# Optimization experiments

Hardware: AMD Instinct MI355X
Metric: run time of the kernel (lower is better)

Reference implementation:

```python
import jax, jax.numpy as jnp
import numpy as np
import math


def _sinusoidal_pe(seq_len, hidden_dim, dtype):
    pos = jnp.arange(seq_len, dtype=jnp.float32)[:, None]              # [S,1]
    div = jnp.exp(jnp.arange(0, hidden_dim, 2, dtype=jnp.float32) * (-math.log(10000.0) / hidden_dim))  # [H/2]
    ang = pos * div                                                    # [S,H/2]
    pe = jnp.stack([jnp.sin(ang), jnp.cos(ang)], axis=-1).reshape(seq_len, hidden_dim)  # interleave sin/cos
    return pe.astype(dtype)


def setup_inputs() -> dict:
    key = jax.random.key(0)
    ks = jax.random.split(key, 12)
    B, S, H = 4, 2048, 1024
    scale = 1.0 / math.sqrt(H)
    inp = {
        "x": jax.random.normal(ks[0], (B, S, H), dtype=jnp.float32),
        "mask": jax.random.randint(ks[1], (B, S, S), 0, 2, dtype=jnp.int32),
        "Wq": jax.random.normal(ks[2], (H, H), dtype=jnp.float32) * scale,
        "bq": jax.random.normal(ks[3], (H,), dtype=jnp.float32) * 0.02,
        "Wk": jax.random.normal(ks[4], (H, H), dtype=jnp.float32) * scale,
        "bk": jax.random.normal(ks[5], (H,), dtype=jnp.float32) * 0.02,
        "Wv": jax.random.normal(ks[6], (H, H), dtype=jnp.float32) * scale,
        "bv": jax.random.normal(ks[7], (H,), dtype=jnp.float32) * 0.02,
        "pos_bias": jax.random.normal(ks[8], (S, S), dtype=jnp.float32),
        "Wo": jax.random.normal(ks[9], (H, H), dtype=jnp.float32) * scale,
        "bo": jax.random.normal(ks[10], (H,), dtype=jnp.float32) * 0.02,
        "gamma": jnp.ones((H,), dtype=jnp.float32),
        "beta": jnp.zeros((H,), dtype=jnp.float32),
    }
    return inp


def reference(x, mask, Wq, bq, Wk, bk, Wv, bv, pos_bias, Wo, bo, gamma, beta):
    B, S, H = x.shape
    scale = math.sqrt(H)
    pe = _sinusoidal_pe(S, H, x.dtype)                  # [S,H]
    xp = x + pe[None, :, :]                             # [B,S,H]
    # torch Linear: y = x @ W.T + b
    q = jnp.einsum('bsh,oh->bso', xp, Wq) + bq
    k = jnp.einsum('bsh,oh->bso', xp, Wk) + bk
    v = jnp.einsum('bsh,oh->bso', xp, Wv) + bv
    scores = jnp.einsum('bqh,bkh->bqk', q, k) / scale   # [B,S,S]
    scores = scores + pos_bias[None, :S, :S]
    scores = jnp.where(mask == 0, jnp.asarray(-1e9, scores.dtype), scores)
    attn = jax.nn.softmax(scores, axis=-1)              # dropout = identity (eval mode)
    context = jnp.einsum('bqk,bkh->bqh', attn, v)
    out = jnp.einsum('bsh,oh->bso', context, Wo) + bo
    # LayerNorm(out + x)
    h = out + x
    mu = jnp.mean(h, axis=-1, keepdims=True)
    var = jnp.var(h, axis=-1, keepdims=True)
    normed = (h - mu) * jax.lax.rsqrt(var + 1e-5) * gamma + beta
    return normed, attn
```

## Files before the change

### kernel.cpp

```cpp
#include <hip/hip_runtime.h>
#include <hip/hip_bf16.h>
#include <math.h>

typedef __hip_bfloat16 bf16;
typedef __bf16 bf16x8 __attribute__((ext_vector_type(8)));
typedef float f32x4 __attribute__((ext_vector_type(4)));

static constexpr int  B_  = 4, S_ = 2048, H_ = 1024;
static constexpr long BSH = (long)B_ * S_ * H_;
static constexpr long SH  = (long)S_ * H_;
static constexpr long SS  = (long)S_ * S_;
static constexpr long HH  = (long)H_ * H_;

#define GLOAD_LDS16(gp, lp)                                                          \
  __builtin_amdgcn_global_load_lds((__attribute__((address_space(1))) void*)(gp),    \
                                   (__attribute__((address_space(3))) void*)(lp),    \
                                   16, 0, 0)

#define BARRIER() do { __builtin_amdgcn_s_barrier(); asm volatile("" ::: "memory"); } while (0)

template <int N> __device__ __forceinline__ void waitcnt_vm() {
  if constexpr (N == 0)      asm volatile("s_waitcnt vmcnt(0)" ::: "memory");
  else if constexpr (N == 8) asm volatile("s_waitcnt vmcnt(8)" ::: "memory");
}

__device__ __forceinline__ float wave_reduce_sum(float v) {
#pragma unroll
  for (int o = 32; o; o >>= 1) v += __shfl_xor(v, o, 64);
  return v;
}
__device__ __forceinline__ float bf16r(float v) {
  return __bfloat162float(__float2bfloat16(v));
}


__device__ __forceinline__ void prep_core(
    int bx, const float* Wq, const float* Wk, const float* Wv, const float* Wo,
    bf16* wdst, const float* x, bf16* xpb,
    const int* mask, unsigned* mask_bits, const float* pos_bias, bf16* pbb) {
  const int tid = threadIdx.x;
  if (bx < 4096) {
    const int w = bx >> 10;
    const float* src = (w == 0) ? Wq : (w == 1) ? Wk : (w == 2) ? Wv : Wo;
    bf16* d = wdst + (long)w * HH;
    const int idx = ((bx & 1023) << 8) + tid;
    const float4 f = ((const float4*)src)[idx];
    d[idx * 4 + 0] = __float2bfloat16(f.x);
    d[idx * 4 + 1] = __float2bfloat16(f.y);
    d[idx * 4 + 2] = __float2bfloat16(f.z);
    d[idx * 4 + 3] = __float2bfloat16(f.w);
  } else if (bx < 20480) {
    const long idx = (((long)(bx - 4096)) << 8) + tid;
    const int  i   = (int)(idx & (H_ / 2 - 1));
    const long bs  = idx >> 9;
    const int  s   = (int)(bs & (S_ - 1));
    const float div = __expf((float)(2 * i) * (-9.210340371976184f / (float)H_));
    const float ang = (float)s * div;
    const float2 xv = ((const float2*)x)[idx];
    xpb[idx * 2 + 0] = __float2bfloat16(xv.x + __sinf(ang));
    xpb[idx * 2 + 1] = __float2bfloat16(xv.y + __cosf(ang));
  } else if (bx < 22528) {
    const long uidx = (((long)(bx - 20480)) << 8) + tid;
    const int4* mp  = (const int4*)mask + uidx * 8;
    unsigned bits = 0;
#pragma unroll
    for (int q = 0; q < 8; ++q) {
      const int4 v = mp[q];
      bits |= (v.x ? 1u : 0u) << (q * 4 + 0);
      bits |= (v.y ? 1u : 0u) << (q * 4 + 1);
      bits |= (v.z ? 1u : 0u) << (q * 4 + 2);
      bits |= (v.w ? 1u : 0u) << (q * 4 + 3);
    }
    mask_bits[uidx] = bits;
  } else {
    const long idx = (((long)(bx - 22528)) << 8) + tid;
    const float4 f = ((const float4*)pos_bias)[idx];
    bf16* d = pbb + idx * 4;
    d[0] = __float2bfloat16(f.x);
    d[1] = __float2bfloat16(f.y);
    d[2] = __float2bfloat16(f.z);
    d[3] = __float2bfloat16(f.w);
  }
}

template <int MODE, bool DBUF>
__device__ __forceinline__ void gemm_core(
    bf16* As, bf16* Bs, int bxx, int byy, int z,
    const bf16* A, long sA, const bf16* Bm, long sB,
    bf16* Cb, float* Cf, long sC, int M, int N, int K,
    const float* bias0, const float* bias1,
    const bf16* pbb, const unsigned* mask_bits,
    const float* xres, const float* inv_sum) {
  constexpr int BM = 128, BN = 128, BK = 64;
  constexpr int TILE = BM * BK;

  const int tid  = threadIdx.x;
  const int lane = tid & 63;
  const int wave = tid >> 6;
  const int wm   = wave & 1;
  const int wn   = wave >> 1;
  const int m0   = bxx * BM;
  const int n0   = byy * BN;

  const bf16* Ab = A  + (long)z * sA;
  const bf16* Bb = Bm + (long)z * sB;

  const int rw = tid >> 3;
  const int cp = (tid & 7) ^ (rw & 7);
  const bf16* ga = Ab + (long)(m0 + rw) * K + cp * 8;
  const bf16* gb = Bb + (long)(n0 + rw) * K + cp * 8;

  auto stage = [&](int tile, int buf) {
    const long k0 = (long)tile * BK;
#pragma unroll
    for (int q = 0; q < 4; ++q) {
      GLOAD_LDS16(ga + (long)(32 * q) * K + k0, As + buf * TILE + tid * 8 + q * 2048);
      GLOAD_LDS16(gb + (long)(32 * q) * K + k0, Bs + buf * TILE + tid * 8 + q * 2048);
    }
  };

  f32x4 acc[4][4] = {};

  const int fr     = lane & 15;
  const int k0slot = lane >> 4;
  const int sw     = fr & 7;

  auto tile_compute = [&](const char* bAc, const char* bBc) {
#pragma unroll
    for (int ks = 0; ks < 2; ++ks) {
      const int co = ((k0slot + 4 * ks) ^ sw) << 4;
      bf16x8 af[4], bfv[4];
#pragma unroll
      for (int i = 0; i < 4; ++i) {
        af[i]  = *(const bf16x8*)(bAc + (wm * 64 + i * 16 + fr) * 128 + co);
        bfv[i] = *(const bf16x8*)(bBc + (wn * 64 + i * 16 + fr) * 128 + co);
      }
#pragma unroll
      for (int i = 0; i < 4; ++i)
#pragma unroll
        for (int j = 0; j < 4; ++j)
          acc[i][j] = __builtin_amdgcn_mfma_f32_16x16x32_bf16(af[i], bfv[j], acc[i][j], 0, 0, 0);
    }
  };

  const int nkt = K / BK;
  if constexpr (DBUF) {
    stage(0, 0);
    for (int kt = 0; kt < nkt; ++kt) {
      const int cur = kt & 1;
      if (kt + 1 < nkt) {
        stage(kt + 1, cur ^ 1);
        waitcnt_vm<8>();
      } else {
        waitcnt_vm<0>();
      }
      BARRIER();
      tile_compute((const char*)(As + cur * TILE), (const char*)(Bs + cur * TILE));
      BARRIER();
    }
  } else {
    for (int kt = 0; kt < nkt; ++kt) {
      stage(kt, 0);
      __syncthreads();
      tile_compute((const char*)As, (const char*)Bs);
      __syncthreads();
    }
  }

  const float* biasz = (MODE == 0) ? ((z == 0) ? bias0 : bias1) : bias0;
  const int cc = lane & 15;
  const int cr = (lane >> 4) * 4;
#pragma unroll
  for (int i = 0; i < 4; ++i) {
    const int rowb = m0 + wm * 64 + i * 16 + cr;
#pragma unroll
    for (int j = 0; j < 4; ++j) {
      const int col = n0 + wn * 64 + j * 16 + cc;
#pragma unroll
      for (int r = 0; r < 4; ++r) {
        const int  row  = rowb + r;
        const long loff = (long)row * N + col;
        const long off  = (long)z * sC + loff;
        const float v   = acc[i][j][r];
        if (MODE == 0) {
          float o = v + biasz[col];
          if (z == 0) o *= 0.03125f;
          Cb[off] = __float2bfloat16(o);
        } else if (MODE == 1) {
          const unsigned mw = mask_bits[off >> 5];
          float sc = v + __bfloat162float(pbb[loff]);
          if (((mw >> (col & 31)) & 1u) == 0u) sc = -1e9f;
          Cb[off] = __float2bfloat16(__expf(fminf(sc, 60.0f)));
        } else if (MODE == 2) {
          Cb[off] = __float2bfloat16(v * inv_sum[z * S_ + row]);
        } else if (MODE == 3) {
          Cf[off] = v + biasz[col] + xres[off];
        } else {
          Cb[off] = __float2bfloat16(v + bias0[row]);
        }
      }
    }
  }
}


__global__ void prep_kernel(const float* __restrict__ Wq, const float* __restrict__ Wk,
                            const float* __restrict__ Wv, const float* __restrict__ Wo,
                            bf16* __restrict__ wdst,
                            const float* __restrict__ x, bf16* __restrict__ xpb,
                            const int* __restrict__ mask, unsigned* __restrict__ mask_bits,
                            const float* __restrict__ pos_bias, bf16* __restrict__ pbb) {
  prep_core(blockIdx.x, Wq, Wk, Wv, Wo, wdst, x, xpb, mask, mask_bits, pos_bias, pbb);
}

__global__ void qkvt_kernel(const bf16* __restrict__ xpb, const bf16* __restrict__ wts,
                            bf16* __restrict__ q_b, bf16* __restrict__ vT,
                            const float* __restrict__ bq, const float* __restrict__ bk,
                            const float* __restrict__ bv) {
  __shared__ bf16 As[128 * 64];
  __shared__ bf16 Bs[128 * 64];
  const int vb = blockIdx.x;
  if (vb < 1024) {
    const int bx = vb & 63, by = (vb >> 6) & 7, z = vb >> 9;
    gemm_core<0, false>(As, Bs, bx, by, z, xpb, 0, wts, HH,
                        q_b, nullptr, BSH, B_ * S_, H_, H_,
                        bq, bk, nullptr, nullptr, nullptr, nullptr);
  } else {
    const int w = vb - 1024, bx = w & 7, by = (w >> 3) & 15, z = w >> 7;
    gemm_core<4, false>(As, Bs, bx, by, z, wts + 2 * HH, 0, xpb, SH,
                        vT, nullptr, SH, H_, S_, H_,
                        bv, nullptr, nullptr, nullptr, nullptr, nullptr);
  }
}

template <int MODE, bool DBUF>
__global__ void gemm_nt(const bf16* __restrict__ A, long sA,
                        const bf16* __restrict__ Bm, long sB,
                        bf16* __restrict__ Cb, float* __restrict__ Cf, long sC,
                        int M, int N, int K,
                        const float* __restrict__ bias0,
                        const float* __restrict__ bias1,
                        const bf16* __restrict__ pbb,
                        const unsigned* __restrict__ mask_bits,
                        const float* __restrict__ xres,
                        const float* __restrict__ inv_sum) {
  constexpr int NBUF = DBUF ? 2 : 1;
  __shared__ bf16 As[NBUF * 128 * 64];
  __shared__ bf16 Bs[NBUF * 128 * 64];
  gemm_core<MODE, DBUF>(As, Bs, blockIdx.x, blockIdx.y, blockIdx.z,
                        A, sA, Bm, sB, Cb, Cf, sC, M, N, K,
                        bias0, bias1, pbb, mask_bits, xres, inv_sum);
}

__global__ void rownorm_kernel(const bf16* __restrict__ E, float* __restrict__ attn_f,
                               float* __restrict__ inv_sum) {
  const long row = blockIdx.x;
  const int  tid = threadIdx.x;
  const uint4 d = *(const uint4*)(E + row * (long)S_ + tid * 8);
  float ev[8];
  ev[0] = __uint_as_float(d.x << 16); ev[1] = __uint_as_float(d.x & 0xffff0000u);
  ev[2] = __uint_as_float(d.y << 16); ev[3] = __uint_as_float(d.y & 0xffff0000u);
  ev[4] = __uint_as_float(d.z << 16); ev[5] = __uint_as_float(d.z & 0xffff0000u);
  ev[6] = __uint_as_float(d.w << 16); ev[7] = __uint_as_float(d.w & 0xffff0000u);
  float s = 0.f;
#pragma unroll
  for (int i = 0; i < 8; ++i) s += ev[i];
  s = wave_reduce_sum(s);
  __shared__ float red[4];
  if ((tid & 63) == 0) red[tid >> 6] = s;
  __syncthreads();
  const float inv = 1.0f / fmaxf(red[0] + red[1] + red[2] + red[3], 1e-30f);
  if (tid == 0) inv_sum[row] = inv;
  float4 o0, o1;
  o0.x = bf16r(ev[0] * inv); o0.y = bf16r(ev[1] * inv);
  o0.z = bf16r(ev[2] * inv); o0.w = bf16r(ev[3] * inv);
  o1.x = bf16r(ev[4] * inv); o1.y = bf16r(ev[5] * inv);
  o1.z = bf16r(ev[6] * inv); o1.w = bf16r(ev[7] * inv);
  float4* dst = (float4*)(attn_f + row * (long)S_ + tid * 8);
  dst[0] = o0;
  dst[1] = o1;
}

__global__ void ln_kernel(float* __restrict__ h, const float* __restrict__ gamma,
                          const float* __restrict__ beta) {
  const long row = blockIdx.x;
  float* hr = h + row * (long)H_;
  const int tid = threadIdx.x;
  const float4 v4 = ((const float4*)hr)[tid];
  float s = v4.x + v4.y + v4.z + v4.w;
  s = wave_reduce_sum(s);
  __shared__ float redA[4], redB[4];
  if ((tid & 63) == 0) redA[tid >> 6] = s;
  __syncthreads();
  const float mu = (redA[0] + redA[1] + redA[2] + redA[3]) * (1.0f / H_);
  const float dx = v4.x - mu, dy = v4.y - mu, dz = v4.z - mu, dw = v4.w - mu;
  float vs = dx * dx + dy * dy + dz * dz + dw * dw;
  vs = wave_reduce_sum(vs);
  if ((tid & 63) == 0) redB[tid >> 6] = vs;
  __syncthreads();
  const float var  = (redB[0] + redB[1] + redB[2] + redB[3]) * (1.0f / H_);
  const float rstd = rsqrtf(var + 1e-5f);
  const float4 g4 = ((const float4*)gamma)[tid];
  const float4 b4 = ((const float4*)beta)[tid];
  float4 o;
  o.x = bf16r(dx * rstd * g4.x + b4.x);
  o.y = bf16r(dy * rstd * g4.y + b4.y);
  o.z = bf16r(dz * rstd * g4.z + b4.z);
  o.w = bf16r(dw * rstd * g4.w + b4.w);
  ((float4*)hr)[tid] = o;
}

extern "C" void kernel_launch(void* const* d_in, const int* in_sizes, int n_in,
                              void* d_out, int out_size, void* d_ws, size_t ws_size,
                              hipStream_t stream) {
  const float* x        = (const float*)d_in[0];
  const int*   mask     = (const int*)d_in[1];
  const float* Wq       = (const float*)d_in[2];
  const float* bq       = (const float*)d_in[3];
  const float* Wk       = (const float*)d_in[4];
  const float* bk       = (const float*)d_in[5];
  const float* Wv       = (const float*)d_in[6];
  const float* bv       = (const float*)d_in[7];
  const float* pos_bias = (const float*)d_in[8];
  const float* Wo       = (const float*)d_in[9];
  const float* bo       = (const float*)d_in[10];
  const float* gamma    = (const float*)d_in[11];
  const float* beta     = (const float*)d_in[12];

  float* normed_f = (float*)d_out;
  float* attn_f   = (float*)((char*)d_out + ((size_t)32 << 20));

  const size_t MiB = (size_t)1 << 20;
  bf16*     xpb       = (bf16*)d_ws;
  bf16*     q_b       = (bf16*)((char*)d_ws +  16 * MiB);
  bf16*     kbuf      = (bf16*)((char*)d_ws +  32 * MiB);
  bf16*     vT        = (bf16*)((char*)d_ws +  64 * MiB);
  bf16*     ctx       = (bf16*)((char*)d_ws +  80 * MiB);
  bf16*     attn_b    = (bf16*)((char*)d_ws +  96 * MiB);
  bf16*     wts       = (bf16*)((char*)d_ws + 128 * MiB);
  float*    inv_sum   = (float*)((char*)d_ws + 136 * MiB);
  unsigned* mask_bits = (unsigned*)((char*)d_ws + 137 * MiB);
  bf16*     pbb       = (bf16*)((char*)d_ws + 139 * MiB);
  bf16* Wob = wts + 3 * HH;

  const int MQKV = B_ * S_;

  prep_kernel<<<dim3(26624), 256, 0, stream>>>(Wq, Wk, Wv, Wo, wts, x, xpb,
                                               mask, mask_bits, pos_bias, pbb);

  qkvt_kernel<<<dim3(1536), 256, 0, stream>>>(xpb, wts, q_b, vT, bq, bk, bv);

  gemm_nt<1, false><<<dim3(16, 16, B_), 256, 0, stream>>>(q_b, SH, kbuf, SH,
                                                          attn_b, nullptr, SS,
                                                          S_, S_, H_, nullptr, nullptr,
                                                          pbb, mask_bits, nullptr, nullptr);

  rownorm_kernel<<<B_ * S_, 256, 0, stream>>>(attn_b, attn_f, inv_sum);

  gemm_nt<2, true><<<dim3(16, 8, B_), 256, 0, stream>>>(attn_b, SS, vT, SH,
                                                        ctx, nullptr, SH,
                                                        S_, H_, S_, nullptr, nullptr,
                                                        nullptr, nullptr, nullptr, inv_sum);

  gemm_nt<3, false><<<dim3(64, 8, 1), 256, 0, stream>>>(ctx, 0, Wob, 0, nullptr, normed_f, 0,
                                                        MQKV, H_, H_, bo, nullptr,
                                                        nullptr, nullptr, x, nullptr);

  ln_kernel<<<B_ * S_, 256, 0, stream>>>(normed_f, gamma, beta);
}
```

Before: 415.6 us.

## Merge row normalization into attention-V GEMM launch and defer scaling to output projection

The separate rownorm kernel and the attn@V GEMM are combined into one launch. The first 512 blocks compute the unnormalized context GEMM, and the remaining blocks compute the row sums and the normalized fp32 attention output. Because the context GEMM no longer depends on inv_sum, the per-row 1/sum scaling moves to the epilogue of the output-projection GEMM, which is linear in the row scale. This removes a launch boundary and lets the memory-bound normalization overlap with the GEMM. The context GEMM also drops double buffering (DBUF=false), and ctx is now stored unnormalized in bf16, which can change rounding.

```diff
diff --git a/kernel.cpp b/kernel.cpp
--- a/kernel.cpp
+++ b/kernel.cpp
@@ -192,15 +192,42 @@
           if (((mw >> (col & 31)) & 1u) == 0u) sc = -1e9f;
           Cb[off] = __float2bfloat16(__expf(fminf(sc, 60.0f)));
         } else if (MODE == 2) {
-          Cb[off] = __float2bfloat16(v * inv_sum[z * S_ + row]);
+          Cb[off] = __float2bfloat16(v);
         } else if (MODE == 3) {
-          Cf[off] = v + biasz[col] + xres[off];
+          Cf[off] = v * inv_sum[row] + biasz[col] + xres[off];
         } else {
           Cb[off] = __float2bfloat16(v + bias0[row]);
         }
       }
     }
   }
+}
+
+__device__ __forceinline__ void rownorm_core(float* red, long row, const bf16* E,
+                                             float* attn_f, float* inv_sum) {
+  const int tid = threadIdx.x;
+  const uint4 d = *(const uint4*)(E + row * (long)S_ + tid * 8);
+  float ev[8];
+  ev[0] = __uint_as_float(d.x << 16); ev[1] = __uint_as_float(d.x & 0xffff0000u);
+  ev[2] = __uint_as_float(d.y << 16); ev[3] = __uint_as_float(d.y & 0xffff0000u);
+  ev[4] = __uint_as_float(d.z << 16); ev[5] = __uint_as_float(d.z & 0xffff0000u);
+  ev[6] = __uint_as_float(d.w << 16); ev[7] = __uint_as_float(d.w & 0xffff0000u);
+  float s = 0.f;
+#pragma unroll
+  for (int i = 0; i < 8; ++i) s += ev[i];
+  s = wave_reduce_sum(s);
+  if ((tid & 63) == 0) red[tid >> 6] = s;
+  __syncthreads();
+  const float inv = 1.0f / fmaxf(red[0] + red[1] + red[2] + red[3], 1e-30f);
+  if (tid == 0) inv_sum[row] = inv;
+  float4 o0, o1;
+  o0.x = bf16r(ev[0] * inv); o0.y = bf16r(ev[1] * inv);
+  o0.z = bf16r(ev[2] * inv); o0.w = bf16r(ev[3] * inv);
+  o1.x = bf16r(ev[4] * inv); o1.y = bf16r(ev[5] * inv);
+  o1.z = bf16r(ev[6] * inv); o1.w = bf16r(ev[7] * inv);
+  float4* dst = (float4*)(attn_f + row * (long)S_ + tid * 8);
+  dst[0] = o0;
+  dst[1] = o1;
 }
 
 
@@ -233,6 +260,23 @@
   }
 }
 
+__global__ void ctxnorm_kernel(const bf16* __restrict__ attn_b, const bf16* __restrict__ vT,
+                               bf16* __restrict__ ctx, float* __restrict__ attn_f,
+                               float* __restrict__ inv_sum) {
+  __shared__ bf16  As[128 * 64];
+  __shared__ bf16  Bs[128 * 64];
+  __shared__ float red[4];
+  const int vb = blockIdx.x;
+  if (vb < 512) {
+    const int bx = vb & 15, by = (vb >> 4) & 7, z = vb >> 7;
+    gemm_core<2, false>(As, Bs, bx, by, z, attn_b, SS, vT, SH,
+                        ctx, nullptr, SH, S_, H_, S_,
+                        nullptr, nullptr, nullptr, nullptr, nullptr, nullptr);
+  } else {
+    rownorm_core(red, vb - 512, attn_b, attn_f, inv_sum);
+  }
+}
+
 template <int MODE, bool DBUF>
 __global__ void gemm_nt(const bf16* __restrict__ A, long sA,
                         const bf16* __restrict__ Bm, long sB,
@@ -250,35 +294,6 @@
   gemm_core<MODE, DBUF>(As, Bs, blockIdx.x, blockIdx.y, blockIdx.z,
                         A, sA, Bm, sB, Cb, Cf, sC, M, N, K,
                         bias0, bias1, pbb, mask_bits, xres, inv_sum);
-}
-
-__global__ void rownorm_kernel(const bf16* __restrict__ E, float* __restrict__ attn_f,
-                               float* __restrict__ inv_sum) {
-  const long row = blockIdx.x;
-  const int  tid = threadIdx.x;
-  const uint4 d = *(const uint4*)(E + row * (long)S_ + tid * 8);
-  float ev[8];
-  ev[0] = __uint_as_float(d.x << 16); ev[1] = __uint_as_float(d.x & 0xffff0000u);
-  ev[2] = __uint_as_float(d.y << 16); ev[3] = __uint_as_float(d.y & 0xffff0000u);
-  ev[4] = __uint_as_float(d.z << 16); ev[5] = __uint_as_float(d.z & 0xffff0000u);
-  ev[6] = __uint_as_float(d.w << 16); ev[7] = __uint_as_float(d.w & 0xffff0000u);
-  float s = 0.f;
-#pragma unroll
-  for (int i = 0; i < 8; ++i) s += ev[i];
-  s = wave_reduce_sum(s);
-  __shared__ float red[4];
-  if ((tid & 63) == 0) red[tid >> 6] = s;
-  __syncthreads();
-  const float inv = 1.0f / fmaxf(red[0] + red[1] + red[2] + red[3], 1e-30f);
-  if (tid == 0) inv_sum[row] = inv;
-  float4 o0, o1;
-  o0.x = bf16r(ev[0] * inv); o0.y = bf16r(ev[1] * inv);
-  o0.z = bf16r(ev[2] * inv); o0.w = bf16r(ev[3] * inv);
-  o1.x = bf16r(ev[4] * inv); o1.y = bf16r(ev[5] * inv);
-  o1.z = bf16r(ev[6] * inv); o1.w = bf16r(ev[7] * inv);
-  float4* dst = (float4*)(attn_f + row * (long)S_ + tid * 8);
-  dst[0] = o0;
-  dst[1] = o1;
 }
 
 __global__ void ln_kernel(float* __restrict__ h, const float* __restrict__ gamma,
@@ -355,16 +370,12 @@
                                                           S_, S_, H_, nullptr, nullptr,
                                                           pbb, mask_bits, nullptr, nullptr);
 
-  rownorm_kernel<<<B_ * S_, 256, 0, stream>>>(attn_b, attn_f, inv_sum);
-
-  gemm_nt<2, true><<<dim3(16, 8, B_), 256, 0, stream>>>(attn_b, SS, vT, SH,
-                                                        ctx, nullptr, SH,
-                                                        S_, H_, S_, nullptr, nullptr,
-                                                        nullptr, nullptr, nullptr, inv_sum);
+  ctxnorm_kernel<<<dim3(512 + B_ * S_), 256, 0, stream>>>(attn_b, vT, ctx,
+                                                          attn_f, inv_sum);
 
   gemm_nt<3, false><<<dim3(64, 8, 1), 256, 0, stream>>>(ctx, 0, Wob, 0, nullptr, normed_f, 0,
                                                         MQKV, H_, H_, bo, nullptr,
-                                                        nullptr, nullptr, x, nullptr);
+                                                        nullptr, nullptr, x, inv_sum);
 
   ln_kernel<<<B_ * S_, 256, 0, stream>>>(normed_f, gamma, beta);
 }
```

Result: faster. 393.9 us (-5.2%).
